# Kernel tuning notes

Measured on AMD Instinct MI355X. Metric: run time of the kernel, lower is better.

The kernel has to match this reference:

```python
import jax, jax.numpy as jnp
import numpy as np

B, T, D = 2, 1024, 2048
N, K, H = 16, 4, 128          # num_heads, num_kv_heads, head_dim
TC = 1024                     # cached tokens
S = TC + T
MAX_WAVELENGTH = 10000.0
BIG_NEG = -2.3819763e38


def _apply_rope(x, positions):
    """RoPE: positions [B,L] applied to x [B,L,heads,H]."""
    half = x.shape[-1] // 2
    freq_exponents = (2.0 / x.shape[-1]) * jnp.arange(half, dtype=jnp.float32)
    timescale = MAX_WAVELENGTH ** freq_exponents                      # [H/2]
    radians = (positions.astype(jnp.float32)[..., None] / timescale)[..., None, :]  # [B,L,1,H/2]
    sin, cos = jnp.sin(radians), jnp.cos(radians)
    x1, x2 = jnp.split(x, 2, axis=-1)
    res = jnp.concatenate([x1 * cos - x2 * sin, x2 * cos + x1 * sin], axis=-1)
    return res.astype(x.dtype)


def setup_inputs() -> dict:
    key = jax.random.key(0)
    ks = jax.random.split(key, 8)
    x = jax.random.normal(ks[0], (B, T, D), dtype=jnp.float32)
    # new tokens sit right after the cache
    positions = jnp.broadcast_to(TC + jnp.arange(T, dtype=jnp.int32), (B, T))
    # causal mask over [cache + new]: query t may attend to keys s <= TC + t
    s_idx = jnp.arange(S)[None, :]
    t_idx = jnp.arange(T)[:, None]
    attn_mask = jnp.broadcast_to((s_idx <= TC + t_idx)[None, None, :, :], (B, 1, T, S))
    cache_k = jax.random.normal(ks[1], (B, TC, K, H), dtype=jnp.float32)
    cache_v = jax.random.normal(ks[2], (B, TC, K, H), dtype=jnp.float32)
    # lecun-normal-ish fan-in scaling (fan_in = D for projections, N*H for output)
    w_q = jax.random.normal(ks[3], (N, D, H), dtype=jnp.float32) * (D ** -0.5)
    w_kv = jax.random.normal(ks[4], (2, K, D, H), dtype=jnp.float32) * (D ** -0.5)
    w_out = jax.random.normal(ks[5], (N, H, D), dtype=jnp.float32) * ((N * H) ** -0.5)
    return {"x": x, "positions": positions, "attn_mask": attn_mask,
            "cache_k": cache_k, "cache_v": cache_v,
            "w_q": w_q, "w_kv": w_kv, "w_out": w_out}


def reference(x, positions, attn_mask, cache_k, cache_v, w_q, w_kv, w_out):
    dtype = x.dtype
    # projections (GQA path: num_kv_heads != num_heads)
    q = jnp.einsum('BTD,NDH->BTNH', x, w_q.astype(dtype))
    kv = jnp.einsum('BSD,CKDH->CBSKH', x, w_kv.astype(dtype))
    k_new, v_new = kv[0], kv[1]
    # inline RoPE + query scaling
    q = _apply_rope(q, positions) * (H ** -0.5)
    k_new = _apply_rope(k_new, positions)
    # KV-cache concat
    k = jnp.concatenate([cache_k, k_new], axis=1)   # [B,S,K,H]
    v = jnp.concatenate([cache_v, v_new], axis=1)
    # group heads: B T (K G) H -> B T K G H
    G = N // K
    qg = q.reshape(q.shape[0], q.shape[1], K, G, H)
    logits = jnp.einsum('BTKGH,BSKH->BKGTS', qg, k,
                        preferred_element_type=jnp.float32)
    masked = jnp.where(attn_mask[:, :, None, :, :], logits, BIG_NEG)
    probs = jax.nn.softmax(masked, axis=-1).astype(dtype)
    enc = jnp.einsum('BKGTS,BSKH->BTKGH', probs, v)
    enc = enc.reshape(enc.shape[0], enc.shape[1], N, H)  # B T (K G) H
    out = jnp.einsum('BTNH,NHD->BTD', enc, w_out.astype(dtype))
    return out, k, v
```

## Files before the change

kernel.cpp:

```cpp
#include <hip/hip_runtime.h>

#define B_  2
#define T_  1024
#define D_  2048
#define NH  16
#define KH  4
#define HD  128
#define TC_ 1024
#define S_  2048

typedef __bf16 bf16x4v __attribute__((ext_vector_type(4)));
typedef __bf16 bf16x8v __attribute__((ext_vector_type(8)));
typedef float  f32x4v  __attribute__((ext_vector_type(4)));

__device__ __forceinline__ void async_copy16(void* lds, const void* g) {
    __builtin_amdgcn_global_load_lds(
        (__attribute__((address_space(1))) void*)g,
        (__attribute__((address_space(3))) void*)lds, 16, 0, 0);
}

__global__ void prep(const float* __restrict__ x, __bf16* __restrict__ xb,
                     const float4* __restrict__ ck, const float4* __restrict__ cv,
                     float* __restrict__ kout, float* __restrict__ vout,
                     __bf16* __restrict__ kb) {
    int bid = blockIdx.x;
    if (bid < 4096) {
        int i = (bid * 256 + threadIdx.x) * 4;
        float4 v = *(const float4*)(x + i);
        bf16x4v o; o[0]=(__bf16)v.x; o[1]=(__bf16)v.y; o[2]=(__bf16)v.z; o[3]=(__bf16)v.w;
        *(bf16x4v*)(xb + i) = o;
    } else {
        int i = (bid - 4096) * 256 + threadIdx.x;
        int b = i >> 17;
        int r = i & 131071;
        float4 kv = ck[i];
        ((float4*)(kout + (size_t)b * S_ * KH * HD))[r] = kv;
        ((float4*)(vout + (size_t)b * S_ * KH * HD))[r] = cv[i];
        int h4 = r & 31;
        int kh = (r >> 5) & 3;
        int s  = r >> 7;
        bf16x4v o; o[0]=(__bf16)kv.x; o[1]=(__bf16)kv.y; o[2]=(__bf16)kv.z; o[3]=(__bf16)kv.w;
        *(bf16x4v*)(kb + (((size_t)(b * KH + kh) * S_ + s) * HD) + h4 * 4) = o;
    }
}

__global__ void tp_all(const float* __restrict__ wq, const float* __restrict__ wkv,
                       const float* __restrict__ wo, __bf16* __restrict__ wt,
                       __bf16* __restrict__ wot) {
    __shared__ float tile[32][33];
    int bid = blockIdx.x;
    int tx = threadIdx.x, ty = threadIdx.y;
    if (bid < 6144) {
        int zz  = bid >> 8;
        int rem = bid & 255;
        int h0 = (rem & 3) * 32;
        int d0 = (rem >> 2) * 32;
        const float* ip = (zz < 16) ? (wq + (size_t)zz * D_ * HD)
                                    : (wkv + (size_t)(zz - 16) * D_ * HD);
        __bf16* op = wt + (size_t)zz * D_ * HD;
        for (int i = 0; i < 32; i += 8)
            tile[ty + i][tx] = ip[(size_t)(d0 + ty + i) * HD + h0 + tx];
        __syncthreads();
        for (int i = 0; i < 32; i += 8)
            op[(size_t)(h0 + ty + i) * D_ + d0 + tx] = (__bf16)tile[tx][ty + i];
    } else {
        int r2  = bid - 6144;
        int n   = r2 >> 8;
        int rem = r2 & 255;
        int d0 = (rem & 63) * 32;
        int h0 = (rem >> 6) * 32;
        const float* ip = wo + (size_t)n * (HD * D_);
        for (int i = 0; i < 32; i += 8)
            tile[ty + i][tx] = ip[(size_t)(h0 + ty + i) * D_ + d0 + tx];
        __syncthreads();
        for (int i = 0; i < 32; i += 8)
            wot[(size_t)(d0 + ty + i) * (NH * HD) + n * HD + h0 + tx] = (__bf16)tile[tx][ty + i];
    }
}

__global__ void tp_v(const float* __restrict__ vout, __bf16* __restrict__ vtb) {
    __shared__ float tile[32][33];
    int z = blockIdx.z; int b = z / KH, kh = z % KH;
    int h0 = blockIdx.x * 32;
    int s0 = blockIdx.y * 32;
    const float* ip = vout + ((size_t)b * S_ * KH + kh) * HD;
    int tx = threadIdx.x, ty = threadIdx.y;
    for (int i = 0; i < 32; i += 8)
        tile[ty + i][tx] = ip[(size_t)(s0 + ty + i) * (KH * HD) + h0 + tx];
    __syncthreads();
    __bf16* op = vtb + ((size_t)b * KH + kh) * (size_t)HD * S_;
    for (int i = 0; i < 32; i += 8)
        op[(size_t)(h0 + ty + i) * S_ + s0 + tx] = (__bf16)tile[tx][ty + i];
}

__global__ __launch_bounds__(256, 2)
void gemm_qkv(const __bf16* __restrict__ A, const __bf16* __restrict__ BT,
              const int* __restrict__ pos, __bf16* __restrict__ qws,
              float* __restrict__ kout, float* __restrict__ vout,
              __bf16* __restrict__ kb) {
    __shared__ __bf16 As[128 * 64];
    __shared__ __bf16 Bs[128 * 64];
    const int m0 = blockIdx.x * 128, n0 = blockIdx.y * 128;
    const int tid = threadIdx.x;
    const int wave = tid >> 6, lane = tid & 63;
    const int quad = lane >> 4, l16 = lane & 15;
    const int wm = (wave & 1) * 64;
    const int bn0 = (wave >> 1) * 32;
    const int lrow = lane >> 3;
    const int lsw  = (lane & 7) ^ (lrow & 7);

    f32x4v acc[4][4];
    for (int i = 0; i < 4; i++)
        for (int j = 0; j < 4; j++)
            acc[i][j] = (f32x4v){0.f, 0.f, 0.f, 0.f};

    const __bf16* Abase = A + (size_t)m0 * D_;
    const __bf16* Bbase = BT + (size_t)n0 * D_;

    for (int k0 = 0; k0 < D_; k0 += 64) {
        for (int j = 0; j < 4; j++) {
            int r = wave * 32 + j * 8;
            async_copy16(As + (size_t)r * 64,
                         Abase + (size_t)(r + lrow) * D_ + k0 + lsw * 8);
            async_copy16(Bs + (size_t)r * 64,
                         Bbase + (size_t)(r + lrow) * D_ + k0 + lsw * 8);
        }
        __syncthreads();
        for (int ks = 0; ks < 2; ks++) {
            const int ch = ((ks * 4 + quad) ^ (l16 & 7)) * 8;
            bf16x8v a[4], b[4];
            for (int i = 0; i < 4; i++)
                a[i] = *(const bf16x8v*)(As + (wm + i * 16 + l16) * 64 + ch);
            for (int j = 0; j < 4; j++) {
                int bn = bn0 + (j >> 1) * 16 + (j & 1) * 64;
                b[j] = *(const bf16x8v*)(Bs + (bn + l16) * 64 + ch);
            }
            for (int i = 0; i < 4; i++)
                for (int j = 0; j < 4; j++)
                    acc[i][j] = __builtin_amdgcn_mfma_f32_16x16x32_bf16(a[i], b[j], acc[i][j], 0, 0, 0);
        }
        __syncthreads();
    }

    const float RFREQ = 9.210340371976184f / 64.0f;
    const float qscale = 0.08838834764831845f;
    const int head = blockIdx.y;

    if (head < NH) {
        for (int i = 0; i < 4; i++)
            for (int r = 0; r < 4; r++) {
                int row = m0 + wm + i * 16 + quad * 4 + r;
                float p = (float)pos[row];
                size_t qo = ((size_t)row * NH + head) * HD;
                for (int jp = 0; jp < 2; jp++) {
                    int hh = bn0 + jp * 16 + l16;
                    float ang = p * __expf(-(float)hh * RFREQ);
                    float sn, cs; __sincosf(ang, &sn, &cs);
                    float x1 = acc[i][jp * 2][r], x2 = acc[i][jp * 2 + 1][r];
                    qws[qo + hh]      = (__bf16)((x1 * cs - x2 * sn) * qscale);
                    qws[qo + hh + 64] = (__bf16)((x2 * cs + x1 * sn) * qscale);
                }
            }
    } else if (head < NH + KH) {
        int kh = head - NH;
        for (int i = 0; i < 4; i++)
            for (int r = 0; r < 4; r++) {
                int row = m0 + wm + i * 16 + quad * 4 + r;
                int b = row >> 10, t = row & 1023;
                float p = (float)pos[row];
                size_t ko  = ((size_t)(b * S_ + TC_ + t) * KH + kh) * HD;
                size_t kbo = ((size_t)(b * KH + kh) * S_ + TC_ + t) * HD;
                for (int jp = 0; jp < 2; jp++) {
                    int hh = bn0 + jp * 16 + l16;
                    float ang = p * __expf(-(float)hh * RFREQ);
                    float sn, cs; __sincosf(ang, &sn, &cs);
                    float x1 = acc[i][jp * 2][r], x2 = acc[i][jp * 2 + 1][r];
                    float k1 = x1 * cs - x2 * sn, k2 = x2 * cs + x1 * sn;
                    kout[ko + hh]      = k1;
                    kout[ko + hh + 64] = k2;
                    kb[kbo + hh]      = (__bf16)k1;
                    kb[kbo + hh + 64] = (__bf16)k2;
                }
            }
    } else {
        int kh = head - NH - KH;
        for (int i = 0; i < 4; i++)
            for (int r = 0; r < 4; r++) {
                int row = m0 + wm + i * 16 + quad * 4 + r;
                int b = row >> 10, t = row & 1023;
                size_t vo = ((size_t)(b * S_ + TC_ + t) * KH + kh) * HD;
                for (int j = 0; j < 4; j++) {
                    int h = bn0 + (j >> 1) * 16 + (j & 1) * 64 + l16;
                    vout[vo + h] = acc[i][j][r];
                }
            }
    }
}

__global__ __launch_bounds__(256, 2)
void gemm_bt(const __bf16* __restrict__ A, const __bf16* __restrict__ BT,
             float* __restrict__ C, int ldc) {
    __shared__ __bf16 As[128 * 64];
    __shared__ __bf16 Bs[128 * 64];
    const int m0 = blockIdx.x * 128, n0 = blockIdx.y * 128;
    const int tid = threadIdx.x;
    const int wave = tid >> 6, lane = tid & 63;
    const int quad = lane >> 4, l16 = lane & 15;
    const int wm = (wave & 1) * 64, wn = (wave >> 1) * 64;
    const int lrow = lane >> 3;
    const int lsw  = (lane & 7) ^ (lrow & 7);

    f32x4v acc[4][4];
    for (int i = 0; i < 4; i++)
        for (int j = 0; j < 4; j++)
            acc[i][j] = (f32x4v){0.f, 0.f, 0.f, 0.f};

    const __bf16* Abase = A + (size_t)m0 * D_;
    const __bf16* Bbase = BT + (size_t)n0 * D_;

    for (int k0 = 0; k0 < D_; k0 += 64) {
        for (int j = 0; j < 4; j++) {
            int r = wave * 32 + j * 8;
            async_copy16(As + (size_t)r * 64,
                         Abase + (size_t)(r + lrow) * D_ + k0 + lsw * 8);
            async_copy16(Bs + (size_t)r * 64,
                         Bbase + (size_t)(r + lrow) * D_ + k0 + lsw * 8);
        }
        __syncthreads();
        for (int ks = 0; ks < 2; ks++) {
            const int ch = ((ks * 4 + quad) ^ (l16 & 7)) * 8;
            bf16x8v a[4], b[4];
            for (int i = 0; i < 4; i++)
                a[i] = *(const bf16x8v*)(As + (wm + i * 16 + l16) * 64 + ch);
            for (int j = 0; j < 4; j++)
                b[j] = *(const bf16x8v*)(Bs + (wn + j * 16 + l16) * 64 + ch);
            for (int i = 0; i < 4; i++)
                for (int j = 0; j < 4; j++)
                    acc[i][j] = __builtin_amdgcn_mfma_f32_16x16x32_bf16(a[i], b[j], acc[i][j], 0, 0, 0);
        }
        __syncthreads();
    }
    for (int i = 0; i < 4; i++)
        for (int j = 0; j < 4; j++)
            for (int r = 0; r < 4; r++) {
                int row = m0 + wm + i * 16 + quad * 4 + r;
                int col = n0 + wn + j * 16 + l16;
                C[(size_t)row * ldc + col] = acc[i][j][r];
            }
}

__global__ __launch_bounds__(512, 1)
void attn(const __bf16* __restrict__ qws, const __bf16* __restrict__ kb,
          const __bf16* __restrict__ vtb, __bf16* __restrict__ enc) {
    __shared__ __bf16 Qs[128 * 128];
    __shared__ __bf16 Ks[128 * 128];
    __shared__ __bf16 Vs[128 * 128];
    __shared__ __bf16 Ps[128 * 128];

    const int t0 = blockIdx.x * 128;
    const int n  = blockIdx.y;
    const int b  = blockIdx.z;
    const int kh = n / (NH / KH);
    const int tid = threadIdx.x, wave = tid >> 6, lane = tid & 63;
    const int quad = lane >> 4, l16 = lane & 15;
    const int wm = wave * 16;
    const int arow = lane >> 4;
    const int acol = lane & 15;

    {
        const __bf16* qtile = qws + ((size_t)(b * T_ + t0) * NH + n) * HD;
        for (int jj = 0; jj < 4; jj++) {
            int r0 = wm + jj * 4;
            int row = r0 + arow;
            async_copy16(Qs + (size_t)r0 * 128,
                         qtile + (size_t)row * (NH * HD) + ((acol ^ (row & 15)) * 8));
        }
    }

    float m_run[4], l_run[4];
    f32x4v o_acc[8];
    for (int r = 0; r < 4; r++) { m_run[r] = -INFINITY; l_run[r] = 0.f; }
    for (int j = 0; j < 8; j++) o_acc[j] = (f32x4v){0.f, 0.f, 0.f, 0.f};

    const int nS = (TC_ + t0 + 128) >> 7;
    const __bf16* kbase = kb  + ((size_t)(b * KH + kh)) * S_ * HD;
    const __bf16* vbase = vtb + ((size_t)(b * KH + kh)) * (size_t)HD * S_;

    for (int st = 0; st < nS; st++) {
        const int s0 = st * 128;
        {
            const __bf16* ktile = kbase + (size_t)s0 * HD;
            for (int jj = 0; jj < 4; jj++) {
                int r0 = wm + jj * 4;
                int row = r0 + arow;
                async_copy16(Ks + (size_t)r0 * 128,
                             ktile + (size_t)row * HD + ((acol ^ (row & 15)) * 8));
            }
        }
        {
            const __bf16* vtile = vbase + s0;
            for (int jj = 0; jj < 4; jj++) {
                int r0 = wm + jj * 4;
                int row = r0 + arow;
                async_copy16(Vs + (size_t)r0 * 128,
                             vtile + (size_t)row * S_ + ((acol ^ (row & 15)) * 8));
            }
        }
        __syncthreads();

        f32x4v sc[8];
        for (int j = 0; j < 8; j++) sc[j] = (f32x4v){0.f, 0.f, 0.f, 0.f};
        for (int ks = 0; ks < 4; ks++) {
            int ch = (ks * 4 + quad) ^ l16;
            bf16x8v a = *(const bf16x8v*)(Qs + (wm + l16) * 128 + ch * 8);
            bf16x8v bb[8];
            for (int j = 0; j < 8; j++)
                bb[j] = *(const bf16x8v*)(Ks + (j * 16 + l16) * 128 + ch * 8);
            for (int j = 0; j < 8; j++)
                sc[j] = __builtin_amdgcn_mfma_f32_16x16x32_bf16(a, bb[j], sc[j], 0, 0, 0);
        }

        if (st == nS - 1) {
            for (int j = 0; j < 8; j++)
                for (int r = 0; r < 4; r++) {
                    int row = wm + quad * 4 + r;
                    int col = j * 16 + l16;
                    if (col > row) sc[j][r] = -3.0e38f;
                }
        }

        for (int r = 0; r < 4; r++) {
            float mx = sc[0][r];
            for (int j = 1; j < 8; j++) mx = fmaxf(mx, sc[j][r]);
            for (int off = 8; off >= 1; off >>= 1) mx = fmaxf(mx, __shfl_xor(mx, off, 64));
            float m;
            if (mx > m_run[r] + 8.f) {
                m = mx;
                float alpha = __expf(m_run[r] - mx);
                for (int j = 0; j < 8; j++) o_acc[j][r] *= alpha;
                l_run[r] *= alpha;
                m_run[r] = m;
            } else {
                m = m_run[r];
            }
            float s = 0.f;
            for (int j = 0; j < 8; j++) {
                float pv = __expf(sc[j][r] - m);
                sc[j][r] = pv;
                s += pv;
            }
            for (int off = 8; off >= 1; off >>= 1) s += __shfl_xor(s, off, 64);
            l_run[r] += s;
        }

        for (int j = 0; j < 8; j++)
            for (int r = 0; r < 4; r++) {
                int row = wm + quad * 4 + r;
                int c = (j * 2 + (l16 >> 3)) ^ (row & 15);
                Ps[row * 128 + c * 8 + (l16 & 7)] = (__bf16)sc[j][r];
            }
        __syncthreads();

        for (int ks = 0; ks < 4; ks++) {
            int ch = (ks * 4 + quad) ^ l16;
            bf16x8v a = *(const bf16x8v*)(Ps + (wm + l16) * 128 + ch * 8);
            bf16x8v bb[8];
            for (int j = 0; j < 8; j++)
                bb[j] = *(const bf16x8v*)(Vs + (j * 16 + l16) * 128 + ch * 8);
            for (int j = 0; j < 8; j++)
                o_acc[j] = __builtin_amdgcn_mfma_f32_16x16x32_bf16(a, bb[j], o_acc[j], 0, 0, 0);
        }
        __syncthreads();
    }

    for (int r = 0; r < 4; r++) {
        float inv = 1.0f / l_run[r];
        int row = wm + quad * 4 + r;
        for (int j = 0; j < 8; j++) {
            int col = j * 16 + l16;
            enc[((size_t)(b * T_ + t0 + row) * NH + n) * HD + col] =
                (__bf16)(o_acc[j][r] * inv);
        }
    }
}

extern "C" void kernel_launch(void* const* d_in, const int* in_sizes, int n_in,
                              void* d_out, int out_size, void* d_ws, size_t ws_size,
                              hipStream_t stream) {
    const float* x       = (const float*)d_in[0];
    const int*   pos     = (const int*)d_in[1];
    const float* cache_k = (const float*)d_in[3];
    const float* cache_v = (const float*)d_in[4];
    const float* w_q     = (const float*)d_in[5];
    const float* w_kv    = (const float*)d_in[6];
    const float* w_out   = (const float*)d_in[7];

    float* out  = (float*)d_out;
    float* kout = out  + (size_t)B_ * T_ * D_;
    float* vout = kout + (size_t)B_ * S_ * KH * HD;

    char* ws = (char*)d_ws;
    __bf16* xb   = (__bf16*)ws;  ws += (size_t)B_ * T_ * D_ * 2;
    __bf16* wt   = (__bf16*)ws;  ws += (size_t)3072 * D_ * 2;
    __bf16* wot  = (__bf16*)ws;  ws += (size_t)D_ * NH * HD * 2;
    __bf16* qws  = (__bf16*)ws;  ws += (size_t)B_ * T_ * NH * HD * 2;
    __bf16* kbuf = (__bf16*)ws;  ws += (size_t)B_ * S_ * KH * HD * 2;
    __bf16* vtb  = (__bf16*)ws;  ws += (size_t)B_ * S_ * KH * HD * 2;
    __bf16* enc  = (__bf16*)ws;

    prep<<<5120, 256, 0, stream>>>(x, xb, (const float4*)cache_k, (const float4*)cache_v,
                                   kout, vout, kbuf);
    tp_all<<<10240, dim3(32, 8), 0, stream>>>(w_q, w_kv, w_out, wt, wot);
    gemm_qkv<<<dim3(16, 24), 256, 0, stream>>>(xb, wt, pos, qws, kout, vout, kbuf);
    tp_v<<<dim3(4, 64, 8), dim3(32, 8), 0, stream>>>(vout, vtb);
    attn<<<dim3(8, 16, 2), 512, 0, stream>>>(qws, kbuf, vtb, enc);
    gemm_bt<<<dim3(16, 16), 256, 0, stream>>>(enc, wot, out, 2048);
}
```

Measured before the change: 275.5 us.

## Split attention waves into 4x2 row/column grid with Q in registers and merge partial softmax

Reorganizes the attention kernel so each wave owns 32 query rows and half of the 128 key columns, instead of 16 rows and all columns. Q is loaded straight into registers rather than staged in LDS, so K fragments are reused across two row fragments. Each column half keeps its own running softmax state, and the two partial results are merged through LDS at the end. The online-softmax lazy-rescale threshold is dropped in favour of an unconditional rescale. The trade-off is more accumulator registers per wave plus a final cross-wave reduction step.

```diff
diff --git a/kernel.cpp b/kernel.cpp
--- a/kernel.cpp
+++ b/kernel.cpp
@@ -252,7 +252,6 @@
 __global__ __launch_bounds__(512, 1)
 void attn(const __bf16* __restrict__ qws, const __bf16* __restrict__ kb,
           const __bf16* __restrict__ vtb, __bf16* __restrict__ enc) {
-    __shared__ __bf16 Qs[128 * 128];
     __shared__ __bf16 Ks[128 * 128];
     __shared__ __bf16 Vs[128 * 128];
     __shared__ __bf16 Ps[128 * 128];
@@ -263,28 +262,34 @@
     const int kh = n / (NH / KH);
     const int tid = threadIdx.x, wave = tid >> 6, lane = tid & 63;
     const int quad = lane >> 4, l16 = lane & 15;
+    const int wr = (wave & 3) * 32;
+    const int wc = (wave >> 2) * 64;
     const int wm = wave * 16;
     const int arow = lane >> 4;
     const int acol = lane & 15;
 
-    {
-        const __bf16* qtile = qws + ((size_t)(b * T_ + t0) * NH + n) * HD;
-        for (int jj = 0; jj < 4; jj++) {
-            int r0 = wm + jj * 4;
-            int row = r0 + arow;
-            async_copy16(Qs + (size_t)r0 * 128,
-                         qtile + (size_t)row * (NH * HD) + ((acol ^ (row & 15)) * 8));
-        }
-    }
-
-    float m_run[4], l_run[4];
-    f32x4v o_acc[8];
-    for (int r = 0; r < 4; r++) { m_run[r] = -INFINITY; l_run[r] = 0.f; }
-    for (int j = 0; j < 8; j++) o_acc[j] = (f32x4v){0.f, 0.f, 0.f, 0.f};
-
-    const int nS = (TC_ + t0 + 128) >> 7;
     const __bf16* kbase = kb  + ((size_t)(b * KH + kh)) * S_ * HD;
     const __bf16* vbase = vtb + ((size_t)(b * KH + kh)) * (size_t)HD * S_;
+
+    bf16x8v qreg[2][4];
+#pragma unroll
+    for (int f = 0; f < 2; f++) {
+        const __bf16* qrow = qws + ((size_t)(b * T_ + t0 + wr + f * 16 + l16) * NH + n) * HD;
+#pragma unroll
+        for (int ks = 0; ks < 4; ks++)
+            qreg[f][ks] = *(const bf16x8v*)(qrow + (ks * 4 + quad) * 8);
+    }
+
+    float m_run[2][4], l_run[2][4];
+    f32x4v o_acc[2][8];
+#pragma unroll
+    for (int f = 0; f < 2; f++)
+        for (int r = 0; r < 4; r++) { m_run[f][r] = -INFINITY; l_run[f][r] = 0.f; }
+#pragma unroll
+    for (int f = 0; f < 2; f++)
+        for (int j = 0; j < 8; j++) o_acc[f][j] = (f32x4v){0.f, 0.f, 0.f, 0.f};
+
+    const int nS = (TC_ + t0 + 128) >> 7;
 
     for (int st = 0; st < nS; st++) {
         const int s0 = st * 128;
@@ -308,79 +313,124 @@
         }
         __syncthreads();
 
-        f32x4v sc[8];
-        for (int j = 0; j < 8; j++) sc[j] = (f32x4v){0.f, 0.f, 0.f, 0.f};
+        f32x4v sc[2][4];
+#pragma unroll
+        for (int f = 0; f < 2; f++)
+            for (int j = 0; j < 4; j++) sc[f][j] = (f32x4v){0.f, 0.f, 0.f, 0.f};
+#pragma unroll
         for (int ks = 0; ks < 4; ks++) {
             int ch = (ks * 4 + quad) ^ l16;
-            bf16x8v a = *(const bf16x8v*)(Qs + (wm + l16) * 128 + ch * 8);
+            bf16x8v bb[4];
+#pragma unroll
+            for (int j = 0; j < 4; j++)
+                bb[j] = *(const bf16x8v*)(Ks + (wc + j * 16 + l16) * 128 + ch * 8);
+#pragma unroll
+            for (int f = 0; f < 2; f++)
+#pragma unroll
+                for (int j = 0; j < 4; j++)
+                    sc[f][j] = __builtin_amdgcn_mfma_f32_16x16x32_bf16(qreg[f][ks], bb[j], sc[f][j], 0, 0, 0);
+        }
+
+        if (st == nS - 1) {
+#pragma unroll
+            for (int f = 0; f < 2; f++)
+                for (int j = 0; j < 4; j++)
+                    for (int r = 0; r < 4; r++) {
+                        int row = wr + f * 16 + quad * 4 + r;
+                        int col = wc + j * 16 + l16;
+                        if (col > row) sc[f][j][r] = -3.0e38f;
+                    }
+        }
+
+#pragma unroll
+        for (int f = 0; f < 2; f++) {
+            for (int r = 0; r < 4; r++) {
+                float mx = sc[f][0][r];
+                for (int j = 1; j < 4; j++) mx = fmaxf(mx, sc[f][j][r]);
+                for (int off = 8; off >= 1; off >>= 1) mx = fmaxf(mx, __shfl_xor(mx, off, 64));
+                mx = fmaxf(mx, m_run[f][r]);
+                float alpha = __expf(m_run[f][r] - mx);
+                m_run[f][r] = mx;
+                float s = 0.f;
+                for (int j = 0; j < 4; j++) {
+                    float pv = __expf(sc[f][j][r] - mx);
+                    sc[f][j][r] = pv;
+                    s += pv;
+                }
+                for (int off = 8; off >= 1; off >>= 1) s += __shfl_xor(s, off, 64);
+                l_run[f][r] = l_run[f][r] * alpha + s;
+                for (int j = 0; j < 8; j++) o_acc[f][j][r] *= alpha;
+            }
+            for (int j = 0; j < 4; j++)
+                for (int r = 0; r < 4; r++) {
+                    int row = wr + f * 16 + quad * 4 + r;
+                    int c = ((wc >> 3) + j * 2 + (l16 >> 3)) ^ (row & 15);
+                    Ps[row * 128 + c * 8 + (l16 & 7)] = (__bf16)sc[f][j][r];
+                }
+        }
+        __syncthreads();
+
+#pragma unroll
+        for (int ks = 0; ks < 2; ks++) {
+            int gch = (wc >> 3) + ks * 4 + quad;
+            bf16x8v a0, a1;
+            {
+                int row0 = wr + l16, row1 = wr + 16 + l16;
+                a0 = *(const bf16x8v*)(Ps + row0 * 128 + (gch ^ (row0 & 15)) * 8);
+                a1 = *(const bf16x8v*)(Ps + row1 * 128 + (gch ^ (row1 & 15)) * 8);
+            }
             bf16x8v bb[8];
+#pragma unroll
             for (int j = 0; j < 8; j++)
-                bb[j] = *(const bf16x8v*)(Ks + (j * 16 + l16) * 128 + ch * 8);
-            for (int j = 0; j < 8; j++)
-                sc[j] = __builtin_amdgcn_mfma_f32_16x16x32_bf16(a, bb[j], sc[j], 0, 0, 0);
-        }
-
-        if (st == nS - 1) {
-            for (int j = 0; j < 8; j++)
+                bb[j] = *(const bf16x8v*)(Vs + (j * 16 + l16) * 128 + (gch ^ l16) * 8);
+#pragma unroll
+            for (int j = 0; j < 8; j++) {
+                o_acc[0][j] = __builtin_amdgcn_mfma_f32_16x16x32_bf16(a0, bb[j], o_acc[0][j], 0, 0, 0);
+                o_acc[1][j] = __builtin_amdgcn_mfma_f32_16x16x32_bf16(a1, bb[j], o_acc[1][j], 0, 0, 0);
+            }
+        }
+        __syncthreads();
+    }
+
+    if (wave >= 4) {
+        int w4 = wave - 4;
+        float* obuf = (float*)(w4 < 2 ? Ks : Vs) + (size_t)(w4 & 1) * 4096;
+#pragma unroll
+        for (int f = 0; f < 2; f++)
+            for (int j = 0; j < 8; j++) {
+                int e = f * 8 + j;
+                *(f32x4v*)(obuf + (size_t)lane * 64 + ((e ^ (lane & 15)) << 2)) = o_acc[f][j];
+            }
+        float* mlb = (float*)Ps;
+        if (l16 == 0)
+            for (int f = 0; f < 2; f++)
                 for (int r = 0; r < 4; r++) {
-                    int row = wm + quad * 4 + r;
-                    int col = j * 16 + l16;
-                    if (col > row) sc[j][r] = -3.0e38f;
-                }
-        }
-
-        for (int r = 0; r < 4; r++) {
-            float mx = sc[0][r];
-            for (int j = 1; j < 8; j++) mx = fmaxf(mx, sc[j][r]);
-            for (int off = 8; off >= 1; off >>= 1) mx = fmaxf(mx, __shfl_xor(mx, off, 64));
-            float m;
-            if (mx > m_run[r] + 8.f) {
-                m = mx;
-                float alpha = __expf(m_run[r] - mx);
-                for (int j = 0; j < 8; j++) o_acc[j][r] *= alpha;
-                l_run[r] *= alpha;
-                m_run[r] = m;
-            } else {
-                m = m_run[r];
-            }
-            float s = 0.f;
-            for (int j = 0; j < 8; j++) {
-                float pv = __expf(sc[j][r] - m);
-                sc[j][r] = pv;
-                s += pv;
-            }
-            for (int off = 8; off >= 1; off >>= 1) s += __shfl_xor(s, off, 64);
-            l_run[r] += s;
-        }
-
-        for (int j = 0; j < 8; j++)
-            for (int r = 0; r < 4; r++) {
-                int row = wm + quad * 4 + r;
-                int c = (j * 2 + (l16 >> 3)) ^ (row & 15);
-                Ps[row * 128 + c * 8 + (l16 & 7)] = (__bf16)sc[j][r];
-            }
-        __syncthreads();
-
-        for (int ks = 0; ks < 4; ks++) {
-            int ch = (ks * 4 + quad) ^ l16;
-            bf16x8v a = *(const bf16x8v*)(Ps + (wm + l16) * 128 + ch * 8);
-            bf16x8v bb[8];
-            for (int j = 0; j < 8; j++)
-                bb[j] = *(const bf16x8v*)(Vs + (j * 16 + l16) * 128 + ch * 8);
-            for (int j = 0; j < 8; j++)
-                o_acc[j] = __builtin_amdgcn_mfma_f32_16x16x32_bf16(a, bb[j], o_acc[j], 0, 0, 0);
-        }
-        __syncthreads();
-    }
-
-    for (int r = 0; r < 4; r++) {
-        float inv = 1.0f / l_run[r];
-        int row = wm + quad * 4 + r;
-        for (int j = 0; j < 8; j++) {
-            int col = j * 16 + l16;
-            enc[((size_t)(b * T_ + t0 + row) * NH + n) * HD + col] =
-                (__bf16)(o_acc[j][r] * inv);
-        }
+                    int row = w4 * 32 + f * 16 + quad * 4 + r;
+                    mlb[row * 2]     = m_run[f][r];
+                    mlb[row * 2 + 1] = l_run[f][r];
+                }
+    }
+    __syncthreads();
+    if (wave < 4) {
+        float* obuf = (float*)(wave < 2 ? Ks : Vs) + (size_t)(wave & 1) * 4096;
+        float* mlb = (float*)Ps;
+#pragma unroll
+        for (int f = 0; f < 2; f++)
+            for (int r = 0; r < 4; r++) {
+                int lrow = wr + f * 16 + quad * 4 + r;
+                float m1 = mlb[lrow * 2], l1 = mlb[lrow * 2 + 1];
+                float m0 = m_run[f][r], l0 = l_run[f][r];
+                float M = fmaxf(m0, m1);
+                float a0 = __expf(m0 - M), a1 = __expf(m1 - M);
+                float inv = 1.f / (l0 * a0 + l1 * a1);
+                size_t eo = ((size_t)(b * T_ + t0 + lrow) * NH + n) * HD;
+                for (int j = 0; j < 8; j++) {
+                    int e = f * 8 + j;
+                    f32x4v o1 = *(const f32x4v*)(obuf + (size_t)lane * 64 + ((e ^ (lane & 15)) << 2));
+                    float v = (o_acc[f][j][r] * a0 + o1[r] * a1) * inv;
+                    enc[eo + j * 16 + l16] = (__bf16)v;
+                }
+            }
     }
 }
 
```

Result: slower. 281.6 us (+2.2%).
